# Performance work log

Hardware: AMD Instinct MI355X
Metric: run time of the kernel (lower is better)

The kernel has to match this reference:

```python
import jax, jax.numpy as jnp
import numpy as np

B, S, D = 2, 2048, 2048
H, KVH = 16, 4
HD = D // H  # 128
ROPE_BASE = 10000.0
EPS = 1e-6
QK_GAIN_INIT = 1.5


def _rms_norm(x):
    var = jnp.mean(jnp.square(x), axis=-1, keepdims=True)
    return x * jax.lax.rsqrt(var + EPS)


def _rope_tables(seqlen, head_dim, dtype):
    half = head_dim // 2
    inv_freq = 1.0 / (ROPE_BASE ** (jnp.arange(0, head_dim, 2, dtype=jnp.float32) / head_dim))
    freqs = jnp.outer(jnp.arange(seqlen, dtype=jnp.float32), inv_freq)  # [S, half]
    return jnp.cos(freqs).astype(dtype)[None, None], jnp.sin(freqs).astype(dtype)[None, None]


def _apply_rotary(x, cos, sin):
    half = x.shape[-1] // 2
    x1, x2 = x[..., :half], x[..., half:]
    return jnp.concatenate((x1 * cos + x2 * sin, -x1 * sin + x2 * cos), axis=-1)


def setup_inputs() -> dict:
    key = jax.random.key(0)
    ks = jax.random.split(key, 5)
    scale = 0.02
    return {
        "x": jax.random.normal(ks[0], (B, S, D), dtype=jnp.float32),
        "Wq": jax.random.normal(ks[1], (D, D), dtype=jnp.float32) * scale,
        "Wk": jax.random.normal(ks[2], (KVH * HD, D), dtype=jnp.float32) * scale,
        "Wv": jax.random.normal(ks[3], (KVH * HD, D), dtype=jnp.float32) * scale,
        "Wproj": jax.random.normal(ks[4], (D, D), dtype=jnp.float32) * scale,
        "q_gain": jnp.full((H,), QK_GAIN_INIT, dtype=jnp.float32),
    }


def reference(x, Wq, Wk, Wv, Wproj, q_gain):
    bsz, seqlen, dim = x.shape
    # QKV projections (torch Linear: y = x @ W.T)
    q = (x @ Wq.T).reshape(bsz, seqlen, H, HD).transpose(0, 2, 1, 3)      # [B,H,S,HD]
    k = (x @ Wk.T).reshape(bsz, seqlen, KVH, HD).transpose(0, 2, 1, 3)    # [B,KVH,S,HD]
    v = (x @ Wv.T).reshape(bsz, seqlen, KVH, HD).transpose(0, 2, 1, 3)
    # QK RMSNorm
    q = _rms_norm(q)
    k = _rms_norm(k)
    # RoPE
    cos, sin = _rope_tables(seqlen, HD, q.dtype)
    q = _apply_rotary(q, cos, sin)
    k = _apply_rotary(k, cos, sin)
    # per-head gain on q
    q = q * q_gain[None, :, None, None]
    # GQA: repeat k/v heads
    n_rep = H // KVH
    k = jnp.repeat(k, n_rep, axis=1)  # [B,H,S,HD]
    v = jnp.repeat(v, n_rep, axis=1)
    # causal SDPA, scale = 1/sqrt(head_dim)
    scores = jnp.einsum("bhqd,bhkd->bhqk", q, k) / jnp.sqrt(jnp.float32(HD))
    causal = jnp.tril(jnp.ones((seqlen, seqlen), dtype=bool))
    scores = jnp.where(causal[None, None], scores, jnp.finfo(scores.dtype).min)
    attn = jax.nn.softmax(scores, axis=-1)
    y = jnp.einsum("bhqk,bhkd->bhqd", attn, v)  # [B,H,S,HD]
    y = y.transpose(0, 2, 1, 3).reshape(bsz, seqlen, dim)
    return y @ Wproj.T
```

## Files before the change

### kernel.cpp

```cpp
#include <hip/hip_runtime.h>
#include <hip/hip_bf16.h>

typedef __attribute__((ext_vector_type(8))) short bf16x8;
typedef __attribute__((ext_vector_type(4))) short bf16x4;
typedef __attribute__((ext_vector_type(4))) float f32x4;
typedef unsigned short u16;

#define B_ 2
#define S_ 2048
#define H_ 16
#define KVH_ 4
#define HD_ 128

__device__ __forceinline__ float bf2f(u16 u) { return __uint_as_float(((unsigned)u) << 16); }
__device__ __forceinline__ u16 f2bf(float f) {
  __hip_bfloat16 h = __float2bfloat16(f);
  return *reinterpret_cast<u16*>(&h);
}
__device__ __forceinline__ void gld16(const void* g, void* l) {
  __builtin_amdgcn_global_load_lds((const __attribute__((address_space(1))) void*)g,
                                   (__attribute__((address_space(3))) void*)l, 16, 0, 0);
}

__global__ void detect_kernel(const u16* __restrict__ x, int* __restrict__ flag) {
  __shared__ int tot;
  if (threadIdx.x == 0) tot = 0;
  __syncthreads();
  int cnt = 0;
  for (int i = threadIdx.x; i < 16384; i += 256) {
    unsigned e = (x[i] >> 7) & 0xFF;
    if (e >= 160) cnt++;
  }
  atomicAdd(&tot, cnt);
  __syncthreads();
  if (threadIdx.x == 0) *flag = (tot >= 8) ? 1 : 0;
}

__global__ __launch_bounds__(256) void convert_all_kernel(
    const void* __restrict__ s0, const void* __restrict__ s1, const void* __restrict__ s2,
    const void* __restrict__ s3, const void* __restrict__ s4,
    u16* __restrict__ d0, u16* __restrict__ d1, u16* __restrict__ d2,
    u16* __restrict__ d3, u16* __restrict__ d4, const int* __restrict__ flag) {
  int bb = blockIdx.x;
  const void* src; u16* dst; int base;
  if (bb < 4096)      { src = s0; dst = d0; base = bb; }
  else if (bb < 6144) { src = s1; dst = d1; base = bb - 4096; }
  else if (bb < 6656) { src = s2; dst = d2; base = bb - 6144; }
  else if (bb < 7168) { src = s3; dst = d3; base = bb - 6656; }
  else                { src = s4; dst = d4; base = bb - 7168; }
  int i = (base * 256 + (int)threadIdx.x) * 8;
  if (*flag) {
    const float* s = (const float*)src;
    float4 a = *(const float4*)(s + i);
    float4 b = *(const float4*)(s + i + 4);
    ushort4 o0, o1;
    o0.x = f2bf(a.x); o0.y = f2bf(a.y); o0.z = f2bf(a.z); o0.w = f2bf(a.w);
    o1.x = f2bf(b.x); o1.y = f2bf(b.y); o1.z = f2bf(b.z); o1.w = f2bf(b.w);
    *(ushort4*)(dst + i) = o0;
    *(ushort4*)(dst + i + 4) = o1;
  } else {
    *(uint4*)(dst + i) = *(const uint4*)((const u16*)src + i);
  }
}

__device__ __forceinline__ void stage16(const u16* __restrict__ src, int row0, int K,
                                        int k0, u16* dst, int tid, int wave) {
#pragma unroll
  for (int s = 0; s < 2; ++s) {
    int f = s * 256 + tid, r = f >> 2, kk = (f & 3) << 3;
    gld16(&src[(size_t)(row0 + r) * K + k0 + kk], &dst[(size_t)(s * 256 + wave * 64) * 8]);
  }
}

__device__ __forceinline__ void mfma_tile(const u16* As, const u16* Bs, f32x4 acc[4][4],
                                          int wr, int wc, int l15, int quad) {
  bf16x8 af[4], bfr[4];
#pragma unroll
  for (int i = 0; i < 4; ++i)
    af[i] = *(const bf16x8*)(&As[(wr + i * 16 + l15) * 32 + quad * 8]);
#pragma unroll
  for (int j = 0; j < 4; ++j)
    bfr[j] = *(const bf16x8*)(&Bs[(wc + j * 16 + l15) * 32 + quad * 8]);
#pragma unroll
  for (int i = 0; i < 4; ++i)
#pragma unroll
    for (int j = 0; j < 4; ++j)
      acc[i][j] = __builtin_amdgcn_mfma_f32_16x16x32_bf16(af[i], bfr[j], acc[i][j], 0, 0, 0);
}

__device__ __forceinline__ void gemm_loop(const u16* __restrict__ A, const u16* __restrict__ W,
                                          int m0, int n0, int tid, int wave,
                                          int l15, int quad,
                                          u16* As0, u16* As1, u16* Bs0, u16* Bs1,
                                          f32x4 acc[4][4]) {
  const int wr = (wave >> 1) * 64, wc = (wave & 1) * 64;
  u16* Asb[2] = {As0, As1};
  u16* Bsb[2] = {Bs0, Bs1};
  stage16(A, m0, 2048, 0, As0, tid, wave);
  stage16(W, n0, 2048, 0, Bs0, tid, wave);
  for (int k0 = 0; k0 < 2048; k0 += 32) {
    int cur = (k0 >> 5) & 1;
    __syncthreads();
    if (k0 + 32 < 2048) {
      stage16(A, m0, 2048, k0 + 32, Asb[cur ^ 1], tid, wave);
      stage16(W, n0, 2048, k0 + 32, Bsb[cur ^ 1], tid, wave);
    }
    mfma_tile(Asb[cur], Bsb[cur], acc, wr, wc, l15, quad);
  }
}

__global__ __launch_bounds__(256) void gemm_qkv_kernel(
    const u16* __restrict__ x,
    const u16* __restrict__ Wq, const u16* __restrict__ Wk, const u16* __restrict__ Wv,
    u16* __restrict__ q, u16* __restrict__ k, u16* __restrict__ vt) {
  __shared__ __align__(16) u16 As[2][128 * 32];
  __shared__ __align__(16) u16 Bs[2][128 * 32];
  const int tid = threadIdx.x;
  const int lane = tid & 63, wave = tid >> 6;
  const int l15 = lane & 15, quad = lane >> 4;
  const int wr = (wave >> 1) * 64, wc = (wave & 1) * 64;
  const int tn = blockIdx.x;
  const int m0 = blockIdx.y * 128;
  const u16* Wp; int n0;
  if (tn < 16)      { Wp = Wq; n0 = tn * 128; }
  else if (tn < 20) { Wp = Wk; n0 = (tn - 16) * 128; }
  else              { Wp = Wv; n0 = (tn - 20) * 128; }

  f32x4 acc[4][4] = {};
  gemm_loop(x, Wp, m0, n0, tid, wave, l15, quad, As[0], As[1], Bs[0], Bs[1], acc);

  if (tn < 20) {
    u16* C = (tn < 16) ? q : k;
    int N = (tn < 16) ? 2048 : 512;
#pragma unroll
    for (int i = 0; i < 4; ++i)
#pragma unroll
      for (int j = 0; j < 4; ++j) {
        int row = m0 + wr + i * 16 + quad * 4;
        int col = n0 + wc + j * 16 + l15;
#pragma unroll
        for (int r = 0; r < 4; ++r)
          C[(size_t)(row + r) * N + col] = f2bf(acc[i][j][r]);
      }
  } else {
#pragma unroll
    for (int i = 0; i < 4; ++i)
#pragma unroll
      for (int j = 0; j < 4; ++j) {
        int row = m0 + wr + i * 16 + quad * 4;
        int col = n0 + wc + j * 16 + l15;
        int bb = row >> 11, ss = row & (S_ - 1);
        int kvh = col >> 7, d = col & (HD_ - 1);
        ushort4 pk;
        pk.x = f2bf(acc[i][j][0]); pk.y = f2bf(acc[i][j][1]);
        pk.z = f2bf(acc[i][j][2]); pk.w = f2bf(acc[i][j][3]);
        *(ushort4*)&vt[(((size_t)bb * KVH_ + kvh) * HD_ + d) * S_ + ss] = pk;
      }
  }
}

__global__ __launch_bounds__(256) void gemm_proj_kernel(
    const u16* __restrict__ A, const u16* __restrict__ Wp, void* __restrict__ outp,
    const int* __restrict__ flag) {
  __shared__ __align__(16) u16 As[2][128 * 32];
  __shared__ __align__(16) u16 Bs[2][128 * 32];
  const int tid = threadIdx.x;
  const int lane = tid & 63, wave = tid >> 6;
  const int l15 = lane & 15, quad = lane >> 4;
  const int wr = (wave >> 1) * 64, wc = (wave & 1) * 64;
  const int m0 = blockIdx.y * 128, n0 = blockIdx.x * 128;

  f32x4 acc[4][4] = {};
  gemm_loop(A, Wp, m0, n0, tid, wave, l15, quad, As[0], As[1], Bs[0], Bs[1], acc);

  const int fl = *flag;
#pragma unroll
  for (int i = 0; i < 4; ++i)
#pragma unroll
    for (int j = 0; j < 4; ++j) {
      int row = m0 + wr + i * 16 + quad * 4;
      int col = n0 + wc + j * 16 + l15;
      if (fl) {
        float* Cf = (float*)outp;
#pragma unroll
        for (int r = 0; r < 4; ++r) Cf[(size_t)(row + r) * 2048 + col] = acc[i][j][r];
      } else {
        u16* Cb = (u16*)outp;
#pragma unroll
        for (int r = 0; r < 4; ++r) Cb[(size_t)(row + r) * 2048 + col] = f2bf(acc[i][j][r]);
      }
    }
}

__global__ __launch_bounds__(256) void rope_rms_kernel(u16* __restrict__ x,
                                                       int rows, int nh,
                                                       const void* __restrict__ gain,
                                                       const int* __restrict__ flag) {
  const int fl = *flag;
  int row  = blockIdx.x * 4 + (threadIdx.x >> 6);
  int lane = threadIdx.x & 63;
  if (row >= rows) return;
  int h = row % nh;
  int s = (row / nh) & (S_ - 1);
  u16* p = x + (size_t)row * HD_;
  float x1 = bf2f(p[lane]);
  float x2 = bf2f(p[lane + 64]);
  float ss = x1 * x1 + x2 * x2;
#pragma unroll
  for (int m = 1; m < 64; m <<= 1) ss += __shfl_xor(ss, m, 64);
  float rn = rsqrtf(ss * (1.0f / 128.0f) + 1e-6f);
  x1 *= rn; x2 *= rn;
  float f = exp2f((float)lane * -0.20762050593046f);
  float ang = (float)s * f;
  float sn, cs;
  sincosf(ang, &sn, &cs);
  float o1 = x1 * cs + x2 * sn;
  float o2 = -x1 * sn + x2 * cs;
  if (gain) {
    float g = fl ? ((const float*)gain)[h] : bf2f(((const u16*)gain)[h]);
    o1 *= g; o2 *= g;
  }
  p[lane]      = f2bf(o1);
  p[lane + 64] = f2bf(o2);
}

#define C1_ 0.127517437f
#define C2_ 24.5258157f
__global__ __launch_bounds__(256) void attn_kernel(const u16* __restrict__ Q,
                                                   const u16* __restrict__ Kg,
                                                   const u16* __restrict__ Vt,
                                                   u16* __restrict__ Y) {
  __shared__ __align__(16) u16 Ks[2][64 * 128];
  __shared__ __align__(16) u16 Vs[2][128 * 64];

  const int tid  = threadIdx.x;
  const int lane = tid & 63;
  const int wave = tid >> 6;
  const int l15  = lane & 15;
  const int quad = lane >> 4;

  const int i   = blockIdx.x;
  const int qt  = (i < 256) ? (31 - (i >> 4)) : ((i - 256) >> 4);
  const int id  = i & 15;
  const int b   = id >> 3;
  const int pr  = id & 7;
  const int h0  = pr * 2;
  const int kvh = pr >> 1;
  const int q0  = qt * 64;
  const int qglob = q0 + wave * 16 + l15;

  bf16x8 qfA[4], qfB[4];
#pragma unroll
  for (int kb = 0; kb < 4; ++kb) {
    size_t base = ((size_t)(b * S_ + qglob) * H_ + h0) * HD_ + kb * 32 + quad * 8;
    qfA[kb] = *(const bf16x8*)&Q[base];
    qfB[kb] = *(const bf16x8*)&Q[base + HD_];
  }

  f32x4 yA[8] = {}, yB[8] = {};
  float lA = 0.f, lB = 0.f;

#define STAGE_KV(jj, bi)                                                                 \
  {                                                                                      \
    int kv0p = (jj) * 64;                                                                \
    _Pragma("unroll") for (int it = 0; it < 4; ++it) {                                   \
      int c = it * 256 + tid, r = c >> 4, ccg = (c & 15) ^ (r & 15);                     \
      gld16(&Kg[((size_t)(b * S_ + kv0p + r) * KVH_ + kvh) * HD_ + ccg * 8],             \
            &Ks[bi][(size_t)(it * 256 + wave * 64) * 8]);                                \
    }                                                                                    \
    _Pragma("unroll") for (int it = 0; it < 4; ++it) {                                   \
      int c = it * 256 + tid, r = c >> 3, ccg = (c & 7) ^ (r & 7);                       \
      gld16(&Vt[(((size_t)b * KVH_ + kvh) * HD_ + r) * S_ + kv0p + ccg * 8],             \
            &Vs[bi][(size_t)(it * 256 + wave * 64) * 8]);                                \
    }                                                                                    \
  }

  STAGE_KV(0, 0);

  for (int j = 0; j <= qt; ++j) {
    const int kv0 = j * 64;
    const int cur = j & 1;
    __syncthreads();
    if (j < qt) STAGE_KV(j + 1, cur ^ 1);
    const u16* Ksc = Ks[cur];
    const u16* Vsc = Vs[cur];

    const bool diag = (j == qt);
    bf16x4 pA[4], pB[4];
#pragma unroll
    for (int n = 0; n < 4; ++n) {
      f32x4 a = {0.f, 0.f, 0.f, 0.f}, c2 = {0.f, 0.f, 0.f, 0.f};
      int krow = n * 16 + l15;
      __builtin_amdgcn_s_setprio(1);
#pragma unroll
      for (int kb = 0; kb < 4; ++kb) {
        bf16x8 kf = *(const bf16x8*)&Ksc[krow * 128 + ((kb * 4 + quad) ^ l15) * 8];
        a  = __builtin_amdgcn_mfma_f32_16x16x32_bf16(kf, qfA[kb], a, 0, 0, 0);
        c2 = __builtin_amdgcn_mfma_f32_16x16x32_bf16(kf, qfB[kb], c2, 0, 0, 0);
      }
      __builtin_amdgcn_s_setprio(0);
      bf16x4 ta, tb;
      if (!diag) {
#pragma unroll
        for (int r = 0; r < 4; ++r) {
          float pa = exp2f(a[r] * C1_ - C2_);
          float pb = exp2f(c2[r] * C1_ - C2_);
          lA += pa; lB += pb;
          ta[r] = (short)f2bf(pa);
          tb[r] = (short)f2bf(pb);
        }
      } else {
#pragma unroll
        for (int r = 0; r < 4; ++r) {
          int kv = kv0 + n * 16 + quad * 4 + r;
          bool msk = (kv > qglob);
          float pa = msk ? 0.f : exp2f(a[r] * C1_ - C2_);
          float pb = msk ? 0.f : exp2f(c2[r] * C1_ - C2_);
          lA += pa; lB += pb;
          ta[r] = (short)f2bf(pa);
          tb[r] = (short)f2bf(pb);
        }
      }
      pA[n] = ta; pB[n] = tb;
    }

    __builtin_amdgcn_s_setprio(1);
#pragma unroll
    for (int t = 0; t < 8; ++t) {
      int d = t * 16 + l15;
      int swz = d & 7;
#pragma unroll
      for (int n = 0; n < 4; ++n) {
        bf16x4 va = *(const bf16x4*)&Vsc[(size_t)(d * 8 + ((2 * n + (quad >> 1)) ^ swz)) * 8 +
                                         (quad & 1) * 4];
        yA[t] = __builtin_amdgcn_mfma_f32_16x16x16bf16_1k(va, pA[n], yA[t], 0, 0, 0);
        yB[t] = __builtin_amdgcn_mfma_f32_16x16x16bf16_1k(va, pB[n], yB[t], 0, 0, 0);
      }
    }
    __builtin_amdgcn_s_setprio(0);
  }

  lA += __shfl_xor(lA, 16, 64); lA += __shfl_xor(lA, 32, 64);
  lB += __shfl_xor(lB, 16, 64); lB += __shfl_xor(lB, 32, 64);
  float ia = 1.0f / lA, ib = 1.0f / lB;
  size_t base = ((size_t)(b * S_ + qglob) * H_ + h0) * HD_;
#pragma unroll
  for (int t = 0; t < 8; ++t) {
    int d0 = t * 16 + quad * 4;
    ushort4 oa, ob;
    oa.x = f2bf(yA[t][0] * ia); oa.y = f2bf(yA[t][1] * ia);
    oa.z = f2bf(yA[t][2] * ia); oa.w = f2bf(yA[t][3] * ia);
    ob.x = f2bf(yB[t][0] * ib); ob.y = f2bf(yB[t][1] * ib);
    ob.z = f2bf(yB[t][2] * ib); ob.w = f2bf(yB[t][3] * ib);
    *(ushort4*)&Y[base + d0]       = oa;
    *(ushort4*)&Y[base + HD_ + d0] = ob;
  }
}

extern "C" void kernel_launch(void* const* d_in, const int* in_sizes, int n_in,
                              void* d_out, int out_size, void* d_ws, size_t ws_size,
                              hipStream_t stream) {
  u16* xb  = (u16*)d_ws;
  u16* Wqb = xb  + (size_t)8388608;
  u16* Wkb = Wqb + (size_t)4194304;
  u16* Wvb = Wkb + (size_t)1048576;
  u16* Wpb = Wvb + (size_t)1048576;
  u16* q   = Wpb + (size_t)4194304;
  u16* k   = q   + (size_t)8388608;
  u16* vt  = k   + (size_t)2097152;
  u16* y   = vt  + (size_t)2097152;
  int* flag = (int*)(y + (size_t)8388608);

  detect_kernel<<<1, 256, 0, stream>>>((const u16*)d_in[0], flag);
  convert_all_kernel<<<9216, 256, 0, stream>>>(d_in[0], d_in[1], d_in[2], d_in[3], d_in[4],
                                               xb, Wqb, Wkb, Wvb, Wpb, flag);

  gemm_qkv_kernel<<<dim3(24, 32), 256, 0, stream>>>(xb, Wqb, Wkb, Wvb, q, k, vt);
  rope_rms_kernel<<<65536 / 4, 256, 0, stream>>>(q, 65536, H_, d_in[5], flag);
  rope_rms_kernel<<<16384 / 4, 256, 0, stream>>>(k, 16384, KVH_, nullptr, flag);
  attn_kernel<<<512, 256, 0, stream>>>(q, k, vt, y);
  gemm_proj_kernel<<<dim3(16, 32), 256, 0, stream>>>(y, Wpb, d_out, flag);
}
```

Baseline: 349.4 us.

## Triple-buffer K and split K/V staging with explicit vmcnt waits in attention

The attention kernel now keeps three K buffers and two V buffers. K for tile j+2 and V for tile j+1 are issued at different points in the loop, and completion is tracked with explicit s_waitcnt vmcnt counts and raw s_barrier in place of __syncthreads. The aim is to hide global-to-LDS load latency further ahead of the QK and PV MFMA phases, so PV only waits for V while later K loads stay in flight. It adds LDS usage (an extra 16KB K buffer), which may lower occupancy. It also adds a second barrier per iteration, and correctness now depends on the hand-counted vmcnt values.

```diff
diff --git a/kernel.cpp b/kernel.cpp
--- a/kernel.cpp
+++ b/kernel.cpp
@@ -21,6 +21,18 @@
   __builtin_amdgcn_global_load_lds((const __attribute__((address_space(1))) void*)g,
                                    (__attribute__((address_space(3))) void*)l, 16, 0, 0);
 }
+
+#define WAITV(n)                                                    \
+  do {                                                              \
+    asm volatile("s_waitcnt vmcnt(" #n ")" ::: "memory");           \
+    __builtin_amdgcn_sched_barrier(0);                              \
+  } while (0)
+#define BAR()                                                       \
+  do {                                                              \
+    __builtin_amdgcn_sched_barrier(0);                              \
+    __builtin_amdgcn_s_barrier();                                   \
+    __builtin_amdgcn_sched_barrier(0);                              \
+  } while (0)
 
 __global__ void detect_kernel(const u16* __restrict__ x, int* __restrict__ flag) {
   __shared__ int tot;
@@ -230,7 +242,7 @@
                                                    const u16* __restrict__ Kg,
                                                    const u16* __restrict__ Vt,
                                                    u16* __restrict__ Y) {
-  __shared__ __align__(16) u16 Ks[2][64 * 128];
+  __shared__ __align__(16) u16 Ks[3][64 * 128];
   __shared__ __align__(16) u16 Vs[2][128 * 64];
 
   const int tid  = threadIdx.x;
@@ -256,34 +268,49 @@
     qfA[kb] = *(const bf16x8*)&Q[base];
     qfB[kb] = *(const bf16x8*)&Q[base + HD_];
   }
+  WAITV(0);
 
   f32x4 yA[8] = {}, yB[8] = {};
   float lA = 0.f, lB = 0.f;
 
-#define STAGE_KV(jj, bi)                                                                 \
+#define STAGE_K(jj, dst)                                                                 \
   {                                                                                      \
     int kv0p = (jj) * 64;                                                                \
     _Pragma("unroll") for (int it = 0; it < 4; ++it) {                                   \
       int c = it * 256 + tid, r = c >> 4, ccg = (c & 15) ^ (r & 15);                     \
       gld16(&Kg[((size_t)(b * S_ + kv0p + r) * KVH_ + kvh) * HD_ + ccg * 8],             \
-            &Ks[bi][(size_t)(it * 256 + wave * 64) * 8]);                                \
+            &(dst)[(size_t)(it * 256 + wave * 64) * 8]);                                 \
     }                                                                                    \
+  }
+#define STAGE_V(jj, dst)                                                                 \
+  {                                                                                      \
+    int kv0p = (jj) * 64;                                                                \
     _Pragma("unroll") for (int it = 0; it < 4; ++it) {                                   \
       int c = it * 256 + tid, r = c >> 3, ccg = (c & 7) ^ (r & 7);                       \
       gld16(&Vt[(((size_t)b * KVH_ + kvh) * HD_ + r) * S_ + kv0p + ccg * 8],             \
-            &Vs[bi][(size_t)(it * 256 + wave * 64) * 8]);                                \
+            &(dst)[(size_t)(it * 256 + wave * 64) * 8]);                                 \
     }                                                                                    \
   }
 
-  STAGE_KV(0, 0);
+  u16 *kp0 = Ks[0], *kp1 = Ks[1], *kp2 = Ks[2];
+  u16 *vp0 = Vs[0], *vp1 = Vs[1];
+
+  STAGE_K(0, kp0);
+  STAGE_V(0, vp0);
+  if (qt >= 1) {
+    STAGE_K(1, kp1);
+    WAITV(8);
+  } else {
+    WAITV(4);
+  }
 
   for (int j = 0; j <= qt; ++j) {
     const int kv0 = j * 64;
-    const int cur = j & 1;
-    __syncthreads();
-    if (j < qt) STAGE_KV(j + 1, cur ^ 1);
-    const u16* Ksc = Ks[cur];
-    const u16* Vsc = Vs[cur];
+    BAR();
+    if (j + 1 <= qt) STAGE_V(j + 1, vp1);
+    if (j + 2 <= qt) STAGE_K(j + 2, kp2);
+    const u16* Ksc = kp0;
+    const u16* Vsc = vp0;
 
     const bool diag = (j == qt);
     bf16x4 pA[4], pB[4];
@@ -324,6 +351,11 @@
       pA[n] = ta; pB[n] = tb;
     }
 
+    if (j + 2 <= qt)      WAITV(12);
+    else if (j + 1 <= qt) WAITV(8);
+    else                  WAITV(0);
+    BAR();
+
     __builtin_amdgcn_s_setprio(1);
 #pragma unroll
     for (int t = 0; t < 8; ++t) {
@@ -338,6 +370,14 @@
       }
     }
     __builtin_amdgcn_s_setprio(0);
+
+    if (j < qt) {
+      if (j + 2 <= qt) WAITV(8);
+      else             WAITV(4);
+    }
+
+    u16* kt = kp0; kp0 = kp1; kp1 = kp2; kp2 = kt;
+    u16* vt2 = vp0; vp0 = vp1; vp1 = vt2;
   }
 
   lA += __shfl_xor(lA, 16, 64); lA += __shfl_xor(lA, 32, 64);
```

New measurement: 382.8 us. 9.5% more time.

## Split attention heads across waves with 512-thread blocks and precomputed V offsets

Applied to the files above, without the earlier changes.

The attention block grows from 4 to 8 waves. Each wave now handles one head of the pair for a 16-row query group, where before one wave computed both heads. This halves the per-wave register footprint (accumulators and Q fragments) and doubles the waves sharing each staged K/V tile, aiming for better latency hiding and occupancy. The V swizzle changes to a rotation pattern with offsets computed once per lane, which cuts per-iteration address arithmetic. In exchange, every wave issues its own K and V fragment LDS reads, so LDS read traffic per tile doubles.

```diff
diff --git a/kernel.cpp b/kernel.cpp
--- a/kernel.cpp
+++ b/kernel.cpp
@@ -226,10 +226,10 @@
 
 #define C1_ 0.127517437f
 #define C2_ 24.5258157f
-__global__ __launch_bounds__(256) void attn_kernel(const u16* __restrict__ Q,
-                                                   const u16* __restrict__ Kg,
-                                                   const u16* __restrict__ Vt,
-                                                   u16* __restrict__ Y) {
+__global__ __launch_bounds__(512, 4) void attn_kernel(const u16* __restrict__ Q,
+                                                      const u16* __restrict__ Kg,
+                                                      const u16* __restrict__ Vt,
+                                                      u16* __restrict__ Y) {
   __shared__ __align__(16) u16 Ks[2][64 * 128];
   __shared__ __align__(16) u16 Vs[2][128 * 64];
 
@@ -238,6 +238,8 @@
   const int wave = tid >> 6;
   const int l15  = lane & 15;
   const int quad = lane >> 4;
+  const int hsel = wave & 1;
+  const int qg   = wave >> 1;
 
   const int i   = blockIdx.x;
   const int qt  = (i < 256) ? (31 - (i >> 4)) : ((i - 256) >> 4);
@@ -247,31 +249,35 @@
   const int h0  = pr * 2;
   const int kvh = pr >> 1;
   const int q0  = qt * 64;
-  const int qglob = q0 + wave * 16 + l15;
-
-  bf16x8 qfA[4], qfB[4];
+  const int qglob = q0 + qg * 16 + l15;
+
+  bf16x8 qf[4];
 #pragma unroll
   for (int kb = 0; kb < 4; ++kb) {
-    size_t base = ((size_t)(b * S_ + qglob) * H_ + h0) * HD_ + kb * 32 + quad * 8;
-    qfA[kb] = *(const bf16x8*)&Q[base];
-    qfB[kb] = *(const bf16x8*)&Q[base + HD_];
-  }
-
-  f32x4 yA[8] = {}, yB[8] = {};
-  float lA = 0.f, lB = 0.f;
+    size_t base = ((size_t)(b * S_ + qglob) * H_ + h0 + hsel) * HD_ + kb * 32 + quad * 8;
+    qf[kb] = *(const bf16x8*)&Q[base];
+  }
+
+  int voff[4];
+#pragma unroll
+  for (int n = 0; n < 4; ++n)
+    voff[n] = (((2 * n + (quad >> 1) + l15) & 7) << 3) + ((quad & 1) << 2);
+
+  f32x4 y[8] = {};
+  float l = 0.f;
 
 #define STAGE_KV(jj, bi)                                                                 \
   {                                                                                      \
     int kv0p = (jj) * 64;                                                                \
-    _Pragma("unroll") for (int it = 0; it < 4; ++it) {                                   \
-      int c = it * 256 + tid, r = c >> 4, ccg = (c & 15) ^ (r & 15);                     \
+    _Pragma("unroll") for (int it = 0; it < 2; ++it) {                                   \
+      int c = it * 512 + tid, r = c >> 4, ccg = (c & 15) ^ (r & 15);                     \
       gld16(&Kg[((size_t)(b * S_ + kv0p + r) * KVH_ + kvh) * HD_ + ccg * 8],             \
-            &Ks[bi][(size_t)(it * 256 + wave * 64) * 8]);                                \
+            &Ks[bi][(size_t)(it * 512 + wave * 64) * 8]);                                \
     }                                                                                    \
-    _Pragma("unroll") for (int it = 0; it < 4; ++it) {                                   \
-      int c = it * 256 + tid, r = c >> 3, ccg = (c & 7) ^ (r & 7);                       \
-      gld16(&Vt[(((size_t)b * KVH_ + kvh) * HD_ + r) * S_ + kv0p + ccg * 8],             \
-            &Vs[bi][(size_t)(it * 256 + wave * 64) * 8]);                                \
+    _Pragma("unroll") for (int it = 0; it < 2; ++it) {                                   \
+      int c = it * 512 + tid, r = c >> 3, sg = ((c & 7) - r) & 7;                        \
+      gld16(&Vt[(((size_t)b * KVH_ + kvh) * HD_ + r) * S_ + kv0p + sg * 8],              \
+            &Vs[bi][(size_t)(it * 512 + wave * 64) * 8]);                                \
     }                                                                                    \
   }
 
@@ -283,31 +289,28 @@
     __syncthreads();
     if (j < qt) STAGE_KV(j + 1, cur ^ 1);
     const u16* Ksc = Ks[cur];
-    const u16* Vsc = Vs[cur];
+    const u16* Vl  = Vs[cur] + l15 * 64;
 
     const bool diag = (j == qt);
-    bf16x4 pA[4], pB[4];
+    bf16x4 p[4];
 #pragma unroll
     for (int n = 0; n < 4; ++n) {
-      f32x4 a = {0.f, 0.f, 0.f, 0.f}, c2 = {0.f, 0.f, 0.f, 0.f};
+      f32x4 a = {0.f, 0.f, 0.f, 0.f};
       int krow = n * 16 + l15;
       __builtin_amdgcn_s_setprio(1);
 #pragma unroll
       for (int kb = 0; kb < 4; ++kb) {
         bf16x8 kf = *(const bf16x8*)&Ksc[krow * 128 + ((kb * 4 + quad) ^ l15) * 8];
-        a  = __builtin_amdgcn_mfma_f32_16x16x32_bf16(kf, qfA[kb], a, 0, 0, 0);
-        c2 = __builtin_amdgcn_mfma_f32_16x16x32_bf16(kf, qfB[kb], c2, 0, 0, 0);
+        a = __builtin_amdgcn_mfma_f32_16x16x32_bf16(kf, qf[kb], a, 0, 0, 0);
       }
       __builtin_amdgcn_s_setprio(0);
-      bf16x4 ta, tb;
+      bf16x4 t;
       if (!diag) {
 #pragma unroll
         for (int r = 0; r < 4; ++r) {
           float pa = exp2f(a[r] * C1_ - C2_);
-          float pb = exp2f(c2[r] * C1_ - C2_);
-          lA += pa; lB += pb;
-          ta[r] = (short)f2bf(pa);
-          tb[r] = (short)f2bf(pb);
+          l += pa;
+          t[r] = (short)f2bf(pa);
         }
       } else {
 #pragma unroll
@@ -315,45 +318,35 @@
           int kv = kv0 + n * 16 + quad * 4 + r;
           bool msk = (kv > qglob);
           float pa = msk ? 0.f : exp2f(a[r] * C1_ - C2_);
-          float pb = msk ? 0.f : exp2f(c2[r] * C1_ - C2_);
-          lA += pa; lB += pb;
-          ta[r] = (short)f2bf(pa);
-          tb[r] = (short)f2bf(pb);
+          l += pa;
+          t[r] = (short)f2bf(pa);
         }
       }
-      pA[n] = ta; pB[n] = tb;
+      p[n] = t;
     }
 
     __builtin_amdgcn_s_setprio(1);
 #pragma unroll
     for (int t = 0; t < 8; ++t) {
-      int d = t * 16 + l15;
-      int swz = d & 7;
 #pragma unroll
       for (int n = 0; n < 4; ++n) {
-        bf16x4 va = *(const bf16x4*)&Vsc[(size_t)(d * 8 + ((2 * n + (quad >> 1)) ^ swz)) * 8 +
-                                         (quad & 1) * 4];
-        yA[t] = __builtin_amdgcn_mfma_f32_16x16x16bf16_1k(va, pA[n], yA[t], 0, 0, 0);
-        yB[t] = __builtin_amdgcn_mfma_f32_16x16x16bf16_1k(va, pB[n], yB[t], 0, 0, 0);
+        bf16x4 va = *(const bf16x4*)&Vl[t * 1024 + voff[n]];
+        y[t] = __builtin_amdgcn_mfma_f32_16x16x16bf16_1k(va, p[n], y[t], 0, 0, 0);
       }
     }
     __builtin_amdgcn_s_setprio(0);
   }
 
-  lA += __shfl_xor(lA, 16, 64); lA += __shfl_xor(lA, 32, 64);
-  lB += __shfl_xor(lB, 16, 64); lB += __shfl_xor(lB, 32, 64);
-  float ia = 1.0f / lA, ib = 1.0f / lB;
-  size_t base = ((size_t)(b * S_ + qglob) * H_ + h0) * HD_;
+  l += __shfl_xor(l, 16, 64); l += __shfl_xor(l, 32, 64);
+  float inv = 1.0f / l;
+  size_t base = ((size_t)(b * S_ + qglob) * H_ + h0 + hsel) * HD_;
 #pragma unroll
   for (int t = 0; t < 8; ++t) {
     int d0 = t * 16 + quad * 4;
-    ushort4 oa, ob;
-    oa.x = f2bf(yA[t][0] * ia); oa.y = f2bf(yA[t][1] * ia);
-    oa.z = f2bf(yA[t][2] * ia); oa.w = f2bf(yA[t][3] * ia);
-    ob.x = f2bf(yB[t][0] * ib); ob.y = f2bf(yB[t][1] * ib);
-    ob.z = f2bf(yB[t][2] * ib); ob.w = f2bf(yB[t][3] * ib);
-    *(ushort4*)&Y[base + d0]       = oa;
-    *(ushort4*)&Y[base + HD_ + d0] = ob;
+    ushort4 o;
+    o.x = f2bf(y[t][0] * inv); o.y = f2bf(y[t][1] * inv);
+    o.z = f2bf(y[t][2] * inv); o.w = f2bf(y[t][3] * inv);
+    *(ushort4*)&Y[base + d0] = o;
   }
 }
 
@@ -378,6 +371,6 @@
   gemm_qkv_kernel<<<dim3(24, 32), 256, 0, stream>>>(xb, Wqb, Wkb, Wvb, q, k, vt);
   rope_rms_kernel<<<65536 / 4, 256, 0, stream>>>(q, 65536, H_, d_in[5], flag);
   rope_rms_kernel<<<16384 / 4, 256, 0, stream>>>(k, 16384, KVH_, nullptr, flag);
-  attn_kernel<<<512, 256, 0, stream>>>(q, k, vt, y);
+  attn_kernel<<<512, 512, 0, stream>>>(q, k, vt, y);
   gemm_proj_kernel<<<dim3(16, 32), 256, 0, stream>>>(y, Wpb, d_out, flag);
 }
```

New measurement: 340.5 us. 2.5% less time.
